# Performance work log

Hardware: AMD Instinct MI355X
Metric: run time of the kernel (lower is better)

## Reference

```python
import jax, jax.numpy as jnp
import numpy as np
from math import sqrt

N = 50000      # n_nodes
M = 800000     # n_edges (avg degree 16)
D = 256        # d_Embedding
H = 8          # heads
DK = 32        # per-head key/query dim
DV = 32        # per-head value dim


def setup_inputs() -> dict:
    key = jax.random.key(0)
    ks = jax.random.split(key, 10)
    s = 0.02
    x = jax.random.normal(ks[0], (N, D), dtype=jnp.float32)
    edge_index = jax.random.randint(ks[1], (2, M), 0, N, dtype=jnp.int32)
    # projection weights stored pre-reshaped to (D, H, dhead); equivalent to nn.Linear(D, H*dhead)
    Wk = jax.random.normal(ks[2], (D, H, DK), dtype=jnp.float32) * s
    bk = jax.random.normal(ks[3], (H, DK), dtype=jnp.float32) * s
    Wq = jax.random.normal(ks[4], (D, H, DK), dtype=jnp.float32) * s
    bq = jax.random.normal(ks[5], (H, DK), dtype=jnp.float32) * s
    Wv = jax.random.normal(ks[6], (D, H, DV), dtype=jnp.float32) * s
    bv = jax.random.normal(ks[7], (H, DV), dtype=jnp.float32) * s
    Wagg = jax.random.normal(ks[8], (H * DV, D), dtype=jnp.float32) * s
    bagg = jnp.zeros((D,), dtype=jnp.float32)
    Wff = jax.random.normal(ks[9], (D, D), dtype=jnp.float32) * s
    bff = jnp.zeros((D,), dtype=jnp.float32)
    return {"x": x, "edge_index": edge_index, "Wk": Wk, "bk": bk, "Wq": Wq,
            "bq": bq, "Wv": Wv, "bv": bv, "Wagg": Wagg, "bagg": bagg,
            "Wff": Wff, "bff": bff}


def reference(x, edge_index, Wk, bk, Wq, bq, Wv, bv, Wagg, bagg, Wff, bff):
    recv = edge_index[0]
    send = edge_index[1]
    # per-head projections: (N, H, d)
    K = jnp.einsum('nd,dhk->nhk', x, Wk) + bk
    Q = jnp.einsum('nd,dhk->nhk', x, Wq) + bq
    V = jnp.einsum('nd,dhv->nhv', x, Wv) + bv
    # edge-wise attention logits: (M, H)
    qk = jnp.sum(Q[recv] * K[send], axis=-1)
    # faithful to original: rescale by 3/global_max, then exp
    att = jnp.exp(qk * 3.0 / jnp.max(qk))
    # segment-softmax normalization over edges sharing a receiver
    sums = jax.ops.segment_sum(att, recv, num_segments=N)  # (N, H)
    att = att / sums[recv] / sqrt(DK)
    # weighted scatter-add of sender values: (N, H, DV)
    msg = att[..., None] * V[send]
    out = jax.ops.segment_sum(msg, recv, num_segments=N)
    out = jax.nn.relu(out).reshape(N, H * DV)
    out = jax.nn.relu(out @ Wagg + bagg)
    out = jax.nn.relu(out @ Wff + bff)
    return x + out
```

## Files before the change

### kernel.cpp

```cpp
#include <hip/hip_runtime.h>

#define N_NODES 50000
#define M_EDGES 800000
#define RP 50048

typedef __bf16 bf16x8 __attribute__((ext_vector_type(8)));
typedef __bf16 bf16x4 __attribute__((ext_vector_type(4)));
typedef float  f32x4  __attribute__((ext_vector_type(4)));

static __device__ __forceinline__ unsigned enc_ord(float f) {
    unsigned b = __float_as_uint(f);
    return (b & 0x80000000u) ? ~b : (b | 0x80000000u);
}
static __device__ __forceinline__ float dec_ord(unsigned u) {
    unsigned b = (u & 0x80000000u) ? (u ^ 0x80000000u) : ~u;
    return __uint_as_float(b);
}
static __device__ __forceinline__ float bflo(unsigned u) { return __uint_as_float(u << 16); }
static __device__ __forceinline__ float bfhi(unsigned u) { return __uint_as_float(u & 0xffff0000u); }
static __device__ __forceinline__ unsigned short bfbits(__bf16 b) {
    unsigned short u; __builtin_memcpy(&u, &b, 2); return u;
}

static __device__ __forceinline__ void gload16(const void* g, void* l) {
    __builtin_amdgcn_global_load_lds(
        (const __attribute__((address_space(1))) void*)g,
        (__attribute__((address_space(3))) void*)l, 16, 0, 0);
}

#define STAGE(buf, kk) do {                                                   \
        int ke0 = (kk) + shi * 8;                                             \
        int ke1 = (kk) + (2 + shi) * 8;                                       \
        size_t lo0 = (size_t)(buf) * 32768 + (size_t)tid * 16;                \
        size_t lo1 = lo0 + 4096;                                              \
        gload16(gA0 + ke0, lds0 + lo0);                                       \
        gload16(gA0 + ke1, lds0 + lo1);                                       \
        gload16(gA1 + ke0, lds0 + 8192 + lo0);                                \
        gload16(gA1 + ke1, lds0 + 8192 + lo1);                                \
        gload16(gB0 + ke0, lds0 + 16384 + lo0);                               \
        gload16(gB0 + ke1, lds0 + 16384 + lo1);                               \
        gload16(gB1 + ke0, lds0 + 24576 + lo0);                               \
        gload16(gB1 + ke1, lds0 + 24576 + lo1);                               \
    } while (0)

__global__ __launch_bounds__(256) void prep_kernel(
    const float* __restrict__ Wk, const float* __restrict__ Wq,
    const float* __restrict__ Wv, const float* __restrict__ Wagg,
    const float* __restrict__ Wff,
    const float* __restrict__ bk, const float* __restrict__ bq,
    const float* __restrict__ bv,
    const float* __restrict__ X,
    __bf16* __restrict__ WHq, __bf16* __restrict__ WLq,
    __bf16* __restrict__ WaH, __bf16* __restrict__ WaL,
    __bf16* __restrict__ WfH, __bf16* __restrict__ WfL,
    float* __restrict__ bqkv, __bf16* __restrict__ xh, __bf16* __restrict__ xl,
    int* __restrict__ counts, int* __restrict__ cursor, unsigned* __restrict__ gmax) {
    int gid = blockIdx.x * 256 + threadIdx.x;
    int stride = gridDim.x * 256;
    for (int i = gid; i < 65536; i += stride) {
        int n = i >> 8, k = i & 255;
        size_t src = (size_t)k * 256 + n;
        float v; __bf16 h;
        v = Wk[src];   h = (__bf16)v; WHq[(size_t)n * 256 + k] = h;
                       WLq[(size_t)n * 256 + k] = (__bf16)(v - (float)h);
        v = Wq[src];   h = (__bf16)v; WHq[(size_t)(256 + n) * 256 + k] = h;
                       WLq[(size_t)(256 + n) * 256 + k] = (__bf16)(v - (float)h);
        v = Wv[src];   h = (__bf16)v; WHq[(size_t)(512 + n) * 256 + k] = h;
                       WLq[(size_t)(512 + n) * 256 + k] = (__bf16)(v - (float)h);
        v = Wagg[src]; h = (__bf16)v; WaH[i] = h; WaL[i] = (__bf16)(v - (float)h);
        v = Wff[src];  h = (__bf16)v; WfH[i] = h; WfL[i] = (__bf16)(v - (float)h);
    }
    const size_t nx = (size_t)N_NODES * 256 / 4;
    for (size_t i = gid; i < nx; i += stride) {
        float4 v = *(const float4*)(X + i * 4);
        bf16x4 hh, ll;
        hh[0] = (__bf16)v.x; ll[0] = (__bf16)(v.x - (float)hh[0]);
        hh[1] = (__bf16)v.y; ll[1] = (__bf16)(v.y - (float)hh[1]);
        hh[2] = (__bf16)v.z; ll[2] = (__bf16)(v.z - (float)hh[2]);
        hh[3] = (__bf16)v.w; ll[3] = (__bf16)(v.w - (float)hh[3]);
        *(bf16x4*)(xh + i * 4) = hh;
        *(bf16x4*)(xl + i * 4) = ll;
    }
    for (int i = gid; i < 768; i += stride)
        bqkv[i] = (i < 256) ? bk[i] : ((i < 512) ? bq[i - 256] : bv[i - 512]);
    for (int i = gid; i < N_NODES; i += stride) { counts[i] = 0; cursor[i] = 0; }
    if (gid == 0) *gmax = 0u;
}

__global__ __launch_bounds__(256) void gemm_qkv(
    const __bf16* __restrict__ Ah, const __bf16* __restrict__ Al,
    const __bf16* __restrict__ Bth, const __bf16* __restrict__ Btl,
    const float* __restrict__ bqkv,
    __bf16* __restrict__ Kb, float* __restrict__ Qo, __bf16* __restrict__ Vb) {
    __shared__ __attribute__((aligned(16))) __bf16 sm[2][4][4][128][8];

    const int NB = 2346, q = NB / 8, r = NB % 8;
    int bid = blockIdx.x;
    int xcd = bid & 7, i0 = bid >> 3;
    int logical = (xcd < r ? xcd * (q + 1) : r * (q + 1) + (xcd - r) * q) + i0;
    int by = logical % 6;
    int bx = logical / 6;
    int row0 = bx * 128;
    int n0   = by * 128;

    int tid  = threadIdx.x;
    int lane = tid & 63, wave = tid >> 6;
    int wm = (wave >> 1) * 64, wn = (wave & 1) * 64;

    f32x4 acc[4][4];
    #pragma unroll
    for (int i = 0; i < 4; i++)
        #pragma unroll
        for (int j = 0; j < 4; j++) acc[i][j] = (f32x4)(0.f);

    int srow = tid & 127;
    int shi  = tid >> 7;
    const __bf16* gA0 = Ah  + (size_t)(row0 + srow) * 256;
    const __bf16* gA1 = Al  + (size_t)(row0 + srow) * 256;
    const __bf16* gB0 = Bth + (size_t)(n0 + srow) * 256;
    const __bf16* gB1 = Btl + (size_t)(n0 + srow) * 256;
    char* lds0 = (char*)&sm[0][0][0][0][0];

    STAGE(0, 0);
    __syncthreads();

    int h = lane >> 4;
    int m_base = wm + (lane & 15);
    int n_base = wn + (lane & 15);

    for (int t = 0; t < 8; t++) {
        int cur = t & 1;
        if (t < 7) STAGE(cur ^ 1, (t + 1) * 32);
        bf16x8 ahf[4], alf[4], bhf[4], blf[4];
        #pragma unroll
        for (int mt = 0; mt < 4; mt++) {
            ahf[mt] = *(const bf16x8*)&sm[cur][0][h][m_base + mt * 16][0];
            alf[mt] = *(const bf16x8*)&sm[cur][1][h][m_base + mt * 16][0];
        }
        #pragma unroll
        for (int nt = 0; nt < 4; nt++) {
            bhf[nt] = *(const bf16x8*)&sm[cur][2][h][n_base + nt * 16][0];
            blf[nt] = *(const bf16x8*)&sm[cur][3][h][n_base + nt * 16][0];
        }
        #pragma unroll
        for (int mt = 0; mt < 4; mt++)
            #pragma unroll
            for (int nt = 0; nt < 4; nt++) {
                acc[mt][nt] = __builtin_amdgcn_mfma_f32_16x16x32_bf16(ahf[mt], bhf[nt], acc[mt][nt], 0, 0, 0);
                acc[mt][nt] = __builtin_amdgcn_mfma_f32_16x16x32_bf16(alf[mt], bhf[nt], acc[mt][nt], 0, 0, 0);
                acc[mt][nt] = __builtin_amdgcn_mfma_f32_16x16x32_bf16(ahf[mt], blf[nt], acc[mt][nt], 0, 0, 0);
            }
        __syncthreads();
    }

    #pragma unroll
    for (int mt = 0; mt < 4; mt++) {
        #pragma unroll
        for (int nt = 0; nt < 4; nt++) {
            int cg = n0 + wn + nt * 16 + (lane & 15);
            #pragma unroll
            for (int rr = 0; rr < 4; rr++) {
                int row = row0 + wm + mt * 16 + (lane >> 4) * 4 + rr;
                if (row < N_NODES) {
                    float v = acc[mt][nt][rr] + bqkv[cg];
                    if (cg < 256)      Kb[(size_t)row * 256 + cg] = (__bf16)v;
                    else if (cg < 512) Qo[(size_t)row * 256 + (cg - 256)] = v;
                    else               Vb[(size_t)row * 256 + (cg - 512)] = (__bf16)v;
                }
            }
        }
    }
}

__global__ void hist_kernel(const int* __restrict__ recv, int* __restrict__ counts) {
    int t = blockIdx.x * 256 + threadIdx.x;
    if (t < M_EDGES) atomicAdd(&counts[recv[t]], 1);
}

__global__ void scan_kernel(const int* __restrict__ counts, int* __restrict__ offsets) {
    __shared__ int part[256];
    int t = threadIdx.x;
    const int per = (N_NODES + 255) / 256;
    int start = t * per;
    int end = min(start + per, N_NODES);
    int s = 0;
    for (int i = start; i < end; i++) s += counts[i];
    part[t] = s;
    __syncthreads();
    if (t == 0) {
        int acc = 0;
        for (int i = 0; i < 256; i++) { int v = part[i]; part[i] = acc; acc += v; }
    }
    __syncthreads();
    int acc = part[t];
    for (int i = start; i < end; i++) { offsets[i] = acc; acc += counts[i]; }
    if (end == N_NODES && start < N_NODES) offsets[N_NODES] = acc;
}

__global__ void fill_kernel(const int* __restrict__ recv, const int* __restrict__ send,
                            const int* __restrict__ offsets,
                            int* __restrict__ cursor, int* __restrict__ ssorted,
                            int* __restrict__ rsorted) {
    int t = blockIdx.x * 256 + threadIdx.x;
    if (t < M_EDGES) {
        int r = recv[t];
        int pos = offsets[r] + atomicAdd(&cursor[r], 1);
        ssorted[pos] = send[t];
        rsorted[pos] = r;
    }
}

__global__ __launch_bounds__(256) void qk_csr_kernel(
    const int* __restrict__ ssorted, const int* __restrict__ rsorted,
    const float* __restrict__ Q, const unsigned short* __restrict__ Kb,
    float* __restrict__ qks, unsigned* __restrict__ gmax) {
    int wave_id = (blockIdx.x * 256 + threadIdx.x) >> 6;
    int lane = threadIdx.x & 63;
    int e_slot = lane >> 5;
    int sl = lane & 31;
    const int nwaves = (gridDim.x * 256) >> 6;
    const int npairs = M_EDGES / 2;
    float wmax = -INFINITY;
    for (int pp = wave_id; pp < npairs; pp += 4 * nwaves) {
        int ep[4]; bool valid[4];
        #pragma unroll
        for (int u = 0; u < 4; u++) {
            int p = pp + u * nwaves;
            valid[u] = p < npairs;
            ep[u] = (valid[u] ? p : pp) * 2 + e_slot;
        }
        int si[4], ri[4];
        #pragma unroll
        for (int u = 0; u < 4; u++) { si[u] = ssorted[ep[u]]; ri[u] = rsorted[ep[u]]; }
        uint4 kv[4]; float4 qa[4], qb[4];
        #pragma unroll
        for (int u = 0; u < 4; u++) {
            kv[u] = *(const uint4*)(Kb + (size_t)si[u] * 256 + sl * 8);
            qa[u] = *(const float4*)(Q + (size_t)ri[u] * 256 + sl * 8);
            qb[u] = *(const float4*)(Q + (size_t)ri[u] * 256 + sl * 8 + 4);
        }
        #pragma unroll
        for (int u = 0; u < 4; u++) {
            float d = qa[u].x * bflo(kv[u].x) + qa[u].y * bfhi(kv[u].x)
                    + qa[u].z * bflo(kv[u].y) + qa[u].w * bfhi(kv[u].y)
                    + qb[u].x * bflo(kv[u].z) + qb[u].y * bfhi(kv[u].z)
                    + qb[u].z * bflo(kv[u].w) + qb[u].w * bfhi(kv[u].w);
            d += __shfl_xor(d, 1);
            d += __shfl_xor(d, 2);
            wmax = fmaxf(wmax, d);
            if ((sl & 3) == 0 && valid[u])
                qks[(size_t)ep[u] * 8 + (sl >> 2)] = d;
        }
    }
    wmax = fmaxf(wmax, __shfl_xor(wmax, 1));
    wmax = fmaxf(wmax, __shfl_xor(wmax, 2));
    wmax = fmaxf(wmax, __shfl_xor(wmax, 4));
    wmax = fmaxf(wmax, __shfl_xor(wmax, 8));
    wmax = fmaxf(wmax, __shfl_xor(wmax, 16));
    wmax = fmaxf(wmax, __shfl_xor(wmax, 32));
    if (lane == 0 && wmax > -INFINITY) atomicMax(gmax, enc_ord(wmax));
}

__global__ __launch_bounds__(256) void node_agg_kernel(
    const int* __restrict__ offsets, const int* __restrict__ ssorted,
    const float* __restrict__ qks, const unsigned short* __restrict__ Vb,
    const unsigned* __restrict__ gmax,
    __bf16* __restrict__ msgH, __bf16* __restrict__ msgL) {
    int wave_id = (blockIdx.x * 256 + threadIdx.x) >> 6;
    int lane = threadIdx.x & 63;
    int h = lane >> 3;
    const int nwaves = (gridDim.x * 256) >> 6;
    const int per = (N_NODES + nwaves - 1) / nwaves;
    int n0 = wave_id * per;
    int nend = min(n0 + per, N_NODES);
    float scale = 3.0f / dec_ord(*gmax);
    for (int n = n0; n < nend; n++) {
        int off = offsets[n];
        int deg = offsets[n + 1] - off;
        float sum = 0.f, a0 = 0.f, a1 = 0.f, a2 = 0.f, a3 = 0.f;
        for (int b = 0; b < deg; b += 64) {
            int bn = min(64, deg - b);
            int idxb = ssorted[off + b + min(lane, bn - 1)];
            #define VROW(i) (*(const uint2*)(Vb + \
                (size_t)__shfl(idxb, min((i), bn - 1)) * 256 + lane * 4))
            #define QKL(i) qks[(size_t)(off + b + min((i), bn - 1)) * 8 + h]
            uint2 v0 = VROW(0);
            uint2 v1 = VROW(1);
            float q0 = QKL(0);
            float q1 = QKL(1);
            for (int i = 0; i < bn; i++) {
                uint2 vc = v0; v0 = v1; v1 = VROW(i + 2);
                float qc = q0; q0 = q1; q1 = QKL(i + 2);
                float a = __expf(qc * scale);
                sum += a;
                a0 += a * bflo(vc.x); a1 += a * bfhi(vc.x);
                a2 += a * bflo(vc.y); a3 += a * bfhi(vc.y);
            }
            #undef VROW
            #undef QKL
        }
        float inv = (deg > 0) ? 1.0f / (sum * 5.65685424949238f) : 0.f;
        float r0 = fmaxf(a0 * inv, 0.f), r1 = fmaxf(a1 * inv, 0.f);
        float r2 = fmaxf(a2 * inv, 0.f), r3 = fmaxf(a3 * inv, 0.f);
        bf16x4 hv, lv;
        hv[0] = (__bf16)r0; lv[0] = (__bf16)(r0 - (float)hv[0]);
        hv[1] = (__bf16)r1; lv[1] = (__bf16)(r1 - (float)hv[1]);
        hv[2] = (__bf16)r2; lv[2] = (__bf16)(r2 - (float)hv[2]);
        hv[3] = (__bf16)r3; lv[3] = (__bf16)(r3 - (float)hv[3]);
        *(bf16x4*)(msgH + (size_t)n * 256 + lane * 4) = hv;
        *(bf16x4*)(msgL + (size_t)n * 256 + lane * 4) = lv;
    }
}

__global__ __launch_bounds__(256) void mlp_fused(
    const __bf16* __restrict__ msgH, const __bf16* __restrict__ msgL,
    const __bf16* __restrict__ WaH, const __bf16* __restrict__ WaL,
    const __bf16* __restrict__ WfH, const __bf16* __restrict__ WfL,
    const float* __restrict__ bagg, const float* __restrict__ bff,
    const float* __restrict__ x, float* __restrict__ out) {
    __shared__ __attribute__((aligned(16))) __bf16 sm[2][4][4][128][8];

    int row0 = blockIdx.x * 128;
    int tid  = threadIdx.x;
    int lane = tid & 63, wave = tid >> 6;
    int wm = (wave >> 1) * 64, wn = (wave & 1) * 64;
    int srow = tid & 127;
    int shi  = tid >> 7;
    char* lds0 = (char*)&sm[0][0][0][0][0];
    int h = lane >> 4;
    int m_base = wm + (lane & 15);
    int n_base = wn + (lane & 15);

    f32x4 acc1[2][4][4];
    #pragma unroll
    for (int nh = 0; nh < 2; nh++)
        #pragma unroll
        for (int i = 0; i < 4; i++)
            #pragma unroll
            for (int j = 0; j < 4; j++) acc1[nh][i][j] = (f32x4)(0.f);

    const __bf16* gA0 = msgH + (size_t)(row0 + srow) * 256;
    const __bf16* gA1 = msgL + (size_t)(row0 + srow) * 256;
    const __bf16* gB0;
    const __bf16* gB1;

    #pragma unroll
    for (int nh = 0; nh < 2; nh++) {
        gB0 = WaH + (size_t)(nh * 128 + srow) * 256;
        gB1 = WaL + (size_t)(nh * 128 + srow) * 256;
        STAGE(0, 0);
        __syncthreads();
        for (int t = 0; t < 8; t++) {
            int cur = t & 1;
            if (t < 7) STAGE(cur ^ 1, (t + 1) * 32);
            bf16x8 ahf[4], alf[4], bhf[4], blf[4];
            #pragma unroll
            for (int mt = 0; mt < 4; mt++) {
                ahf[mt] = *(const bf16x8*)&sm[cur][0][h][m_base + mt * 16][0];
                alf[mt] = *(const bf16x8*)&sm[cur][1][h][m_base + mt * 16][0];
            }
            #pragma unroll
            for (int nt = 0; nt < 4; nt++) {
                bhf[nt] = *(const bf16x8*)&sm[cur][2][h][n_base + nt * 16][0];
                blf[nt] = *(const bf16x8*)&sm[cur][3][h][n_base + nt * 16][0];
            }
            #pragma unroll
            for (int mt = 0; mt < 4; mt++)
                #pragma unroll
                for (int nt = 0; nt < 4; nt++) {
                    acc1[nh][mt][nt] = __builtin_amdgcn_mfma_f32_16x16x32_bf16(ahf[mt], bhf[nt], acc1[nh][mt][nt], 0, 0, 0);
                    acc1[nh][mt][nt] = __builtin_amdgcn_mfma_f32_16x16x32_bf16(alf[mt], bhf[nt], acc1[nh][mt][nt], 0, 0, 0);
                    acc1[nh][mt][nt] = __builtin_amdgcn_mfma_f32_16x16x32_bf16(ahf[mt], blf[nt], acc1[nh][mt][nt], 0, 0, 0);
                }
            __syncthreads();
        }
    }

    unsigned hidp[2][4][4][4];
    #pragma unroll
    for (int nh = 0; nh < 2; nh++)
        #pragma unroll
        for (int mt = 0; mt < 4; mt++)
            #pragma unroll
            for (int nt = 0; nt < 4; nt++)
                #pragma unroll
                for (int rr = 0; rr < 4; rr++) {
                    int col = nh * 128 + wn + nt * 16 + (lane & 15);
                    float v = acc1[nh][mt][nt][rr] + bagg[col];
                    v = fmaxf(v, 0.f);
                    __bf16 hh = (__bf16)v;
                    __bf16 hl = (__bf16)(v - (float)hh);
                    hidp[nh][mt][nt][rr] =
                        (unsigned)bfbits(hh) | ((unsigned)bfbits(hl) << 16);
                }

    unsigned short* chunkw = (unsigned short*)lds0;
    const __bf16*   chunkb = (const __bf16*)lds0;
    unsigned short* b2w    = (unsigned short*)(lds0 + 16384);
    const __bf16*   b2b    = (const __bf16*)(lds0 + 16384);

    for (int oh = 0; oh < 2; oh++) {
        f32x4 acc2[4][4];
        #pragma unroll
        for (int i = 0; i < 4; i++)
            #pragma unroll
            for (int j = 0; j < 4; j++) acc2[i][j] = (f32x4)(0.f);

        #pragma unroll
        for (int s = 0; s < 8; s++) {
            __syncthreads();
            int nh = s >> 2, sq = s & 3;
            if (wn == ((sq >= 2) ? 64 : 0)) {
                int nt0 = (sq & 1) * 2;
                #pragma unroll
                for (int mt = 0; mt < 4; mt++)
                    #pragma unroll
                    for (int j = 0; j < 2; j++) {
                        int nt = nt0 + j;
                        int kc = (wn + nt * 16 + (lane & 15)) - 32 * sq;
                        int ks = kc >> 3, e = kc & 7;
                        #pragma unroll
                        for (int rr = 0; rr < 4; rr++) {
                            int row = wm + mt * 16 + (lane >> 4) * 4 + rr;
                            unsigned u = hidp[nh][mt][nt][rr];
                            chunkw[(size_t)ks * 1024 + row * 8 + e] =
                                (unsigned short)(u & 0xffffu);
                            chunkw[(size_t)(4 + ks) * 1024 + row * 8 + e] =
                                (unsigned short)(u >> 16);
                        }
                    }
            }
            {
                int ks0 = shi * 2;
                #pragma unroll
                for (int j = 0; j < 2; j++) {
                    int ks = ks0 + j;
                    gload16(WfH + (size_t)(oh * 128 + srow) * 256 + 32 * s + ks * 8,
                            (char*)b2w + (size_t)ks * 2048 + srow * 16);
                    gload16(WfL + (size_t)(oh * 128 + srow) * 256 + 32 * s + ks * 8,
                            (char*)b2w + (size_t)(4 + ks) * 2048 + srow * 16);
                }
            }
            __syncthreads();
            bf16x8 a2h[4], a2l[4], b2h[4], b2l[4];
            #pragma unroll
            for (int mt = 0; mt < 4; mt++) {
                a2h[mt] = *(const bf16x8*)&chunkb[(size_t)h * 1024 + (m_base + mt * 16) * 8];
                a2l[mt] = *(const bf16x8*)&chunkb[(size_t)(4 + h) * 1024 + (m_base + mt * 16) * 8];
            }
            #pragma unroll
            for (int nt = 0; nt < 4; nt++) {
                b2h[nt] = *(const bf16x8*)&b2b[(size_t)h * 1024 + (n_base + nt * 16) * 8];
                b2l[nt] = *(const bf16x8*)&b2b[(size_t)(4 + h) * 1024 + (n_base + nt * 16) * 8];
            }
            #pragma unroll
            for (int mt = 0; mt < 4; mt++)
                #pragma unroll
                for (int nt = 0; nt < 4; nt++) {
                    acc2[mt][nt] = __builtin_amdgcn_mfma_f32_16x16x32_bf16(a2h[mt], b2h[nt], acc2[mt][nt], 0, 0, 0);
                    acc2[mt][nt] = __builtin_amdgcn_mfma_f32_16x16x32_bf16(a2l[mt], b2h[nt], acc2[mt][nt], 0, 0, 0);
                    acc2[mt][nt] = __builtin_amdgcn_mfma_f32_16x16x32_bf16(a2h[mt], b2l[nt], acc2[mt][nt], 0, 0, 0);
                }
        }
        #pragma unroll
        for (int mt = 0; mt < 4; mt++)
            #pragma unroll
            for (int nt = 0; nt < 4; nt++) {
                int oc = oh * 128 + wn + nt * 16 + (lane & 15);
                #pragma unroll
                for (int rr = 0; rr < 4; rr++) {
                    int row = row0 + wm + mt * 16 + (lane >> 4) * 4 + rr;
                    if (row < N_NODES) {
                        float v = acc2[mt][nt][rr] + bff[oc];
                        v = fmaxf(v, 0.f);
                        size_t idx = (size_t)row * 256 + oc;
                        out[idx] = v + x[idx];
                    }
                }
            }
    }
}

extern "C" void kernel_launch(void* const* d_in, const int* in_sizes, int n_in,
                              void* d_out, int out_size, void* d_ws, size_t ws_size,
                              hipStream_t stream) {
    const float* x    = (const float*)d_in[0];
    const int*   edge = (const int*)d_in[1];
    const int*   recv = edge;
    const int*   send = edge + M_EDGES;
    const float* Wk   = (const float*)d_in[2];
    const float* bk   = (const float*)d_in[3];
    const float* Wq   = (const float*)d_in[4];
    const float* bq   = (const float*)d_in[5];
    const float* Wv   = (const float*)d_in[6];
    const float* bv   = (const float*)d_in[7];
    const float* Wagg = (const float*)d_in[8];
    const float* bagg = (const float*)d_in[9];
    const float* Wff  = (const float*)d_in[10];
    const float* bff  = (const float*)d_in[11];
    float* out = (float*)d_out;

    float*  Qbuf  = (float*)d_ws;
    float*  reg2  = Qbuf + (size_t)RP * 256;
    float*  qks   = reg2 + (size_t)RP * 256;
    __bf16* Kbf   = (__bf16*)(qks + (size_t)M_EDGES * 8);
    __bf16* Vbf   = Kbf + (size_t)RP * 256;
    int* counts   = (int*)(Vbf + (size_t)RP * 256);
    int* cursor   = counts + N_NODES;
    int* offsets  = cursor + N_NODES;
    int* ssorted  = offsets + N_NODES + 1;
    unsigned* gmax = (unsigned*)(ssorted + M_EDGES);
    __bf16* wt    = (__bf16*)(gmax + 1);
    __bf16* WHq = wt;
    __bf16* WLq = wt + 3 * 65536;
    __bf16* WaH = wt + 6 * 65536;  __bf16* WaL = wt + 7 * 65536;
    __bf16* WfH = wt + 8 * 65536;  __bf16* WfL = wt + 9 * 65536;
    float* bqkv = (float*)(wt + 10 * 65536);
    __bf16* xh   = (__bf16*)reg2;
    __bf16* xl   = xh + (size_t)RP * 256;
    int*    rsorted = (int*)reg2;
    __bf16* msgH = (__bf16*)reg2;
    __bf16* msgL = msgH + (size_t)RP * 256;

    dim3 blk(256);
    dim3 edge_grid((M_EDGES + 255) / 256);

    hipLaunchKernelGGL(prep_kernel, dim3(2048), blk, 0, stream,
                       Wk, Wq, Wv, Wagg, Wff, bk, bq, bv, x,
                       WHq, WLq, WaH, WaL, WfH, WfL, bqkv, xh, xl,
                       counts, cursor, gmax);
    hipLaunchKernelGGL(gemm_qkv, dim3(2346), blk, 0, stream,
                       xh, xl, WHq, WLq, bqkv, Kbf, Qbuf, Vbf);
    hipLaunchKernelGGL(hist_kernel, edge_grid, blk, 0, stream, recv, counts);
    hipLaunchKernelGGL(scan_kernel, dim3(1), blk, 0, stream, counts, offsets);
    hipLaunchKernelGGL(fill_kernel, edge_grid, blk, 0, stream, recv, send, offsets,
                       cursor, ssorted, rsorted);
    hipLaunchKernelGGL(qk_csr_kernel, dim3(1024), blk, 0, stream,
                       ssorted, rsorted, Qbuf, (const unsigned short*)Kbf, qks, gmax);
    hipLaunchKernelGGL(node_agg_kernel, dim3(2048), blk, 0, stream,
                       offsets, ssorted, qks, (const unsigned short*)Vbf, gmax,
                       msgH, msgL);
    hipLaunchKernelGGL(mlp_fused, dim3((N_NODES + 127) / 128), blk, 0, stream,
                       msgH, msgL, WaH, WaL, WfH, WfL, bagg, bff, x, out);
}
```

Baseline: 840.3 us.

## Store GEMM operands in pre-tiled panel layout for contiguous LDS staging

Changes the global layout of the bf16 hi/lo copies of x, the weights and the aggregated messages to a panel-tiled format that matches the LDS tile layout (128-row blocks, 32-wide k chunks, 8-element groups). Each staging load then reads a fully contiguous 8 KB span per k-step instead of strided 16-byte pieces from 128 different rows, which should improve global load coalescing in the QKV and MLP GEMMs. In exchange the producer kernels (prep and aggregation) write scattered 8-byte pieces, and every consumer of these buffers must agree on the new layout.

```diff
diff --git a/kernel.cpp b/kernel.cpp
--- a/kernel.cpp
+++ b/kernel.cpp
@@ -22,26 +22,31 @@
     unsigned short u; __builtin_memcpy(&u, &b, 2); return u;
 }
 
+static __device__ __forceinline__ size_t PE(int m, int k) {
+    return (size_t)(m >> 7) * 32768 + (size_t)(k >> 5) * 4096 +
+           (size_t)((k >> 3) & 3) * 1024 + (size_t)(m & 127) * 8 + (k & 7);
+}
+
 static __device__ __forceinline__ void gload16(const void* g, void* l) {
     __builtin_amdgcn_global_load_lds(
         (const __attribute__((address_space(1))) void*)g,
         (__attribute__((address_space(3))) void*)l, 16, 0, 0);
 }
 
-#define STAGE(buf, kk) do {                                                   \
-        int ke0 = (kk) + shi * 8;                                             \
-        int ke1 = (kk) + (2 + shi) * 8;                                       \
-        size_t lo0 = (size_t)(buf) * 32768 + (size_t)tid * 16;                \
-        size_t lo1 = lo0 + 4096;                                              \
-        gload16(gA0 + ke0, lds0 + lo0);                                       \
-        gload16(gA0 + ke1, lds0 + lo1);                                       \
-        gload16(gA1 + ke0, lds0 + 8192 + lo0);                                \
-        gload16(gA1 + ke1, lds0 + 8192 + lo1);                                \
-        gload16(gB0 + ke0, lds0 + 16384 + lo0);                               \
-        gload16(gB0 + ke1, lds0 + 16384 + lo1);                               \
-        gload16(gB1 + ke0, lds0 + 24576 + lo0);                               \
-        gload16(gB1 + ke1, lds0 + 24576 + lo1);                               \
-    } while (0)
+static __device__ __forceinline__ void stage_panel(
+    const char* a0, const char* a1, const char* b0, const char* b1,
+    char* lds0, int buf, int t, int tid) {
+    size_t so = (size_t)t * 8192 + (size_t)tid * 16;
+    size_t lo = (size_t)buf * 32768 + (size_t)tid * 16;
+    gload16(a0 + so, lds0 + lo);
+    gload16(a0 + so + 4096, lds0 + lo + 4096);
+    gload16(a1 + so, lds0 + 8192 + lo);
+    gload16(a1 + so + 4096, lds0 + 8192 + lo + 4096);
+    gload16(b0 + so, lds0 + 16384 + lo);
+    gload16(b0 + so + 4096, lds0 + 16384 + lo + 4096);
+    gload16(b1 + so, lds0 + 24576 + lo);
+    gload16(b1 + so + 4096, lds0 + 24576 + lo + 4096);
+}
 
 __global__ __launch_bounds__(256) void prep_kernel(
     const float* __restrict__ Wk, const float* __restrict__ Wq,
@@ -61,25 +66,29 @@
         int n = i >> 8, k = i & 255;
         size_t src = (size_t)k * 256 + n;
         float v; __bf16 h;
-        v = Wk[src];   h = (__bf16)v; WHq[(size_t)n * 256 + k] = h;
-                       WLq[(size_t)n * 256 + k] = (__bf16)(v - (float)h);
-        v = Wq[src];   h = (__bf16)v; WHq[(size_t)(256 + n) * 256 + k] = h;
-                       WLq[(size_t)(256 + n) * 256 + k] = (__bf16)(v - (float)h);
-        v = Wv[src];   h = (__bf16)v; WHq[(size_t)(512 + n) * 256 + k] = h;
-                       WLq[(size_t)(512 + n) * 256 + k] = (__bf16)(v - (float)h);
-        v = Wagg[src]; h = (__bf16)v; WaH[i] = h; WaL[i] = (__bf16)(v - (float)h);
-        v = Wff[src];  h = (__bf16)v; WfH[i] = h; WfL[i] = (__bf16)(v - (float)h);
+        v = Wk[src];   h = (__bf16)v; WHq[PE(n, k)] = h;
+                       WLq[PE(n, k)] = (__bf16)(v - (float)h);
+        v = Wq[src];   h = (__bf16)v; WHq[PE(n + 256, k)] = h;
+                       WLq[PE(n + 256, k)] = (__bf16)(v - (float)h);
+        v = Wv[src];   h = (__bf16)v; WHq[PE(n + 512, k)] = h;
+                       WLq[PE(n + 512, k)] = (__bf16)(v - (float)h);
+        v = Wagg[src]; h = (__bf16)v; WaH[PE(n, k)] = h;
+                       WaL[PE(n, k)] = (__bf16)(v - (float)h);
+        v = Wff[src];  h = (__bf16)v; WfH[PE(n, k)] = h;
+                       WfL[PE(n, k)] = (__bf16)(v - (float)h);
     }
     const size_t nx = (size_t)N_NODES * 256 / 4;
     for (size_t i = gid; i < nx; i += stride) {
         float4 v = *(const float4*)(X + i * 4);
+        int n = (int)(i >> 6), k0 = (int)((i * 4) & 255);
         bf16x4 hh, ll;
         hh[0] = (__bf16)v.x; ll[0] = (__bf16)(v.x - (float)hh[0]);
         hh[1] = (__bf16)v.y; ll[1] = (__bf16)(v.y - (float)hh[1]);
         hh[2] = (__bf16)v.z; ll[2] = (__bf16)(v.z - (float)hh[2]);
         hh[3] = (__bf16)v.w; ll[3] = (__bf16)(v.w - (float)hh[3]);
-        *(bf16x4*)(xh + i * 4) = hh;
-        *(bf16x4*)(xl + i * 4) = ll;
+        size_t idx = PE(n, k0);
+        *(bf16x4*)(xh + idx) = hh;
+        *(bf16x4*)(xl + idx) = ll;
     }
     for (int i = gid; i < 768; i += stride)
         bqkv[i] = (i < 256) ? bk[i] : ((i < 512) ? bq[i - 256] : bv[i - 512]);
@@ -88,8 +97,8 @@
 }
 
 __global__ __launch_bounds__(256) void gemm_qkv(
-    const __bf16* __restrict__ Ah, const __bf16* __restrict__ Al,
-    const __bf16* __restrict__ Bth, const __bf16* __restrict__ Btl,
+    const __bf16* __restrict__ AhP, const __bf16* __restrict__ AlP,
+    const __bf16* __restrict__ BhP, const __bf16* __restrict__ BlP,
     const float* __restrict__ bqkv,
     __bf16* __restrict__ Kb, float* __restrict__ Qo, __bf16* __restrict__ Vb) {
     __shared__ __attribute__((aligned(16))) __bf16 sm[2][4][4][128][8];
@@ -113,15 +122,13 @@
         #pragma unroll
         for (int j = 0; j < 4; j++) acc[i][j] = (f32x4)(0.f);
 
-    int srow = tid & 127;
-    int shi  = tid >> 7;
-    const __bf16* gA0 = Ah  + (size_t)(row0 + srow) * 256;
-    const __bf16* gA1 = Al  + (size_t)(row0 + srow) * 256;
-    const __bf16* gB0 = Bth + (size_t)(n0 + srow) * 256;
-    const __bf16* gB1 = Btl + (size_t)(n0 + srow) * 256;
+    const char* a0 = (const char*)AhP + (size_t)bx * 65536;
+    const char* a1 = (const char*)AlP + (size_t)bx * 65536;
+    const char* b0 = (const char*)BhP + (size_t)by * 65536;
+    const char* b1 = (const char*)BlP + (size_t)by * 65536;
     char* lds0 = (char*)&sm[0][0][0][0][0];
 
-    STAGE(0, 0);
+    stage_panel(a0, a1, b0, b1, lds0, 0, 0, tid);
     __syncthreads();
 
     int h = lane >> 4;
@@ -130,7 +137,7 @@
 
     for (int t = 0; t < 8; t++) {
         int cur = t & 1;
-        if (t < 7) STAGE(cur ^ 1, (t + 1) * 32);
+        if (t < 7) stage_panel(a0, a1, b0, b1, lds0, cur ^ 1, t + 1, tid);
         bf16x8 ahf[4], alf[4], bhf[4], blf[4];
         #pragma unroll
         for (int mt = 0; mt < 4; mt++) {
@@ -307,25 +314,25 @@
         hv[1] = (__bf16)r1; lv[1] = (__bf16)(r1 - (float)hv[1]);
         hv[2] = (__bf16)r2; lv[2] = (__bf16)(r2 - (float)hv[2]);
         hv[3] = (__bf16)r3; lv[3] = (__bf16)(r3 - (float)hv[3]);
-        *(bf16x4*)(msgH + (size_t)n * 256 + lane * 4) = hv;
-        *(bf16x4*)(msgL + (size_t)n * 256 + lane * 4) = lv;
+        size_t idx = PE(n, lane * 4);
+        *(bf16x4*)(msgH + idx) = hv;
+        *(bf16x4*)(msgL + idx) = lv;
     }
 }
 
 __global__ __launch_bounds__(256) void mlp_fused(
-    const __bf16* __restrict__ msgH, const __bf16* __restrict__ msgL,
-    const __bf16* __restrict__ WaH, const __bf16* __restrict__ WaL,
-    const __bf16* __restrict__ WfH, const __bf16* __restrict__ WfL,
+    const __bf16* __restrict__ msgHP, const __bf16* __restrict__ msgLP,
+    const __bf16* __restrict__ WaHP, const __bf16* __restrict__ WaLP,
+    const __bf16* __restrict__ WfHP, const __bf16* __restrict__ WfLP,
     const float* __restrict__ bagg, const float* __restrict__ bff,
     const float* __restrict__ x, float* __restrict__ out) {
     __shared__ __attribute__((aligned(16))) __bf16 sm[2][4][4][128][8];
 
     int row0 = blockIdx.x * 128;
+    int bxp  = blockIdx.x;
     int tid  = threadIdx.x;
     int lane = tid & 63, wave = tid >> 6;
     int wm = (wave >> 1) * 64, wn = (wave & 1) * 64;
-    int srow = tid & 127;
-    int shi  = tid >> 7;
     char* lds0 = (char*)&sm[0][0][0][0][0];
     int h = lane >> 4;
     int m_base = wm + (lane & 15);
@@ -339,20 +346,18 @@
             #pragma unroll
             for (int j = 0; j < 4; j++) acc1[nh][i][j] = (f32x4)(0.f);
 
-    const __bf16* gA0 = msgH + (size_t)(row0 + srow) * 256;
-    const __bf16* gA1 = msgL + (size_t)(row0 + srow) * 256;
-    const __bf16* gB0;
-    const __bf16* gB1;
+    const char* a0 = (const char*)msgHP + (size_t)bxp * 65536;
+    const char* a1 = (const char*)msgLP + (size_t)bxp * 65536;
 
     #pragma unroll
     for (int nh = 0; nh < 2; nh++) {
-        gB0 = WaH + (size_t)(nh * 128 + srow) * 256;
-        gB1 = WaL + (size_t)(nh * 128 + srow) * 256;
-        STAGE(0, 0);
+        const char* b0 = (const char*)WaHP + (size_t)nh * 65536;
+        const char* b1 = (const char*)WaLP + (size_t)nh * 65536;
+        stage_panel(a0, a1, b0, b1, lds0, 0, 0, tid);
         __syncthreads();
         for (int t = 0; t < 8; t++) {
             int cur = t & 1;
-            if (t < 7) STAGE(cur ^ 1, (t + 1) * 32);
+            if (t < 7) stage_panel(a0, a1, b0, b1, lds0, cur ^ 1, t + 1, tid);
             bf16x8 ahf[4], alf[4], bhf[4], blf[4];
             #pragma unroll
             for (int mt = 0; mt < 4; mt++) {
@@ -396,10 +401,12 @@
 
     unsigned short* chunkw = (unsigned short*)lds0;
     const __bf16*   chunkb = (const __bf16*)lds0;
-    unsigned short* b2w    = (unsigned short*)(lds0 + 16384);
+    char*           b2c    = lds0 + 16384;
     const __bf16*   b2b    = (const __bf16*)(lds0 + 16384);
 
     for (int oh = 0; oh < 2; oh++) {
+        const char* f0 = (const char*)WfHP + (size_t)oh * 65536;
+        const char* f1 = (const char*)WfLP + (size_t)oh * 65536;
         f32x4 acc2[4][4];
         #pragma unroll
         for (int i = 0; i < 4; i++)
@@ -431,15 +438,12 @@
                     }
             }
             {
-                int ks0 = shi * 2;
-                #pragma unroll
-                for (int j = 0; j < 2; j++) {
-                    int ks = ks0 + j;
-                    gload16(WfH + (size_t)(oh * 128 + srow) * 256 + 32 * s + ks * 8,
-                            (char*)b2w + (size_t)ks * 2048 + srow * 16);
-                    gload16(WfL + (size_t)(oh * 128 + srow) * 256 + 32 * s + ks * 8,
-                            (char*)b2w + (size_t)(4 + ks) * 2048 + srow * 16);
-                }
+                size_t so = (size_t)s * 8192 + (size_t)tid * 16;
+                size_t lo = (size_t)tid * 16;
+                gload16(f0 + so, b2c + lo);
+                gload16(f0 + so + 4096, b2c + lo + 4096);
+                gload16(f1 + so, b2c + 8192 + lo);
+                gload16(f1 + so + 4096, b2c + 8192 + lo + 4096);
             }
             __syncthreads();
             bf16x8 a2h[4], a2l[4], b2h[4], b2l[4];
```

Result: no change. 834.1 us (-0.7%).
